# Optimization experiments

Measured on AMD Instinct MI355X. Metric: run time of the kernel, lower is better.

Reference implementation:

```python
import jax, jax.numpy as jnp
import numpy as np

REGION_INDEX = [[3,0,1,2,4],[7,8,9,10,11],[5,6],[13,12],[14,15,23,24,32,33],[22,21,31,30,40,39],[16,17,18,19,20],[25,26,27,28,29],[34,35,36,37,38],[41,42],[49,48],[43,44,45,46,47],[50,51,57],[56,55,61],[52,53,54],[58,59,60]]
INPUT_SIZE = 5
HIDDEN = 100
REGIONS = 16


def setup_inputs() -> dict:
    key = jax.random.key(0)
    ks = jax.random.split(key, 5)
    features = jax.random.normal(ks[0], (128, 256, 62, INPUT_SIZE), dtype=jnp.float32)
    s = 1.0 / np.sqrt(HIDDEN)  # PyTorch LSTM init scale
    # dir 0 = forward, dir 1 = reverse
    w_ih = jax.random.uniform(ks[1], (REGIONS, 2, 4 * HIDDEN, INPUT_SIZE), jnp.float32, -s, s)
    w_hh = jax.random.uniform(ks[2], (REGIONS, 2, 4 * HIDDEN, HIDDEN), jnp.float32, -s, s)
    b_ih = jax.random.uniform(ks[3], (REGIONS, 2, 4 * HIDDEN), jnp.float32, -s, s)
    b_hh = jax.random.uniform(ks[4], (REGIONS, 2, 4 * HIDDEN), jnp.float32, -s, s)
    return {"features": features, "w_ih": w_ih, "w_hh": w_hh, "b_ih": b_ih, "b_hh": b_hh}


def _lstm_last(x, Wih, Whh, bih, bhh):
    # x: (N, L, I) -> final hidden state h_{L-1}: (N, H). PyTorch gate order i,f,g,o.
    N = x.shape[0]
    H = Whh.shape[1]
    bias = bih + bhh

    def step(carry, xt):
        h, c = carry
        g = xt @ Wih.T + h @ Whh.T + bias
        i, f, gg, o = jnp.split(g, 4, axis=-1)
        c = jax.nn.sigmoid(f) * c + jax.nn.sigmoid(i) * jnp.tanh(gg)
        h = jax.nn.sigmoid(o) * jnp.tanh(c)
        return (h, c), None

    h0 = jnp.zeros((N, H), x.dtype)
    (h, _), _ = jax.lax.scan(step, (h0, h0), jnp.swapaxes(x, 0, 1))
    return h


def _forward(features, w_ih, w_hh, b_ih, b_hh):
    # flatten (B, T, 62, 5) -> (N, 62, 5)
    x = features.reshape(-1, features.shape[2], features.shape[3])
    outs = []
    for r in range(REGIONS):
        idx = jnp.asarray(REGION_INDEX[r])
        xr = x[:, idx, :]  # (N, L_r, 5)
        # forward-direction hidden at last timestep
        h_f = _lstm_last(xr, w_ih[r, 0], w_hh[r, 0], b_ih[r, 0], b_hh[r, 0])
        # reverse-direction output at last position == one step on x[:, -1] from zero state
        h_b = _lstm_last(xr[:, -1:, :], w_ih[r, 1], w_hh[r, 1], b_ih[r, 1], b_hh[r, 1])
        outs.append(jnp.concatenate([h_f, h_b], axis=-1))  # (N, 2H)
    return jnp.stack(outs, axis=1)  # (N, 16, 2H)


def reference(features, w_ih, w_hh, b_ih, b_hh):
    return _forward(features, w_ih, w_hh, b_ih, b_hh)
```

## Files before the change

kernel.cpp:

```cpp
#include <hip/hip_runtime.h>


typedef _Float16 f16;
typedef _Float16 half8 __attribute__((ext_vector_type(8)));
typedef float floatx4 __attribute__((ext_vector_type(4)));

#define FEAT_STRIDE 310
#define AST 136
#define OST 104

__constant__ int c_pos[16][6] = {
 {3,0,1,2,4,0},{7,8,9,10,11,0},{5,6,0,0,0,0},{13,12,0,0,0,0},
 {14,15,23,24,32,33},{22,21,31,30,40,39},{16,17,18,19,20,0},{25,26,27,28,29,0},
 {34,35,36,37,38,0},{41,42,0,0,0,0},{49,48,0,0,0,0},{43,44,45,46,47,0},
 {50,51,57,0,0,0},{56,55,61,0,0,0},{52,53,54,0,0,0},{58,59,60,0,0,0}};
__constant__ int c_len[16] = {5,5,2,2,6,6,5,5,5,2,2,5,3,3,3,3};

__device__ __forceinline__ float sigf(float x) {
  return __builtin_amdgcn_rcpf(1.f + __builtin_amdgcn_exp2f(-1.44269504088896f * x));
}
__device__ __forceinline__ float tanhf_fast(float x) {
  return 1.f - 2.f * __builtin_amdgcn_rcpf(1.f + __builtin_amdgcn_exp2f(2.88539008177793f * x));
}

__global__ __launch_bounds__(256) void prep_kernel(
    const float* __restrict__ w_ih, const float* __restrict__ w_hh,
    const float* __restrict__ b_ih, const float* __restrict__ b_hh,
    f16* __restrict__ wp)
{
  int id = blockIdx.x * 256 + threadIdx.x;
  if (id >= 16 * 400 * 128) return;
  int k = id & 127;
  int rowN = (id >> 7) % 400;
  int r = (id >> 7) / 400;
  int j = rowN >> 2, g = rowN & 3;
  int orig = (r * 2 + 0) * 400 + g * 100 + j;
  float v;
  if (k < 100)       v = w_hh[orig * 100 + k];
  else if (k < 105)  v = w_ih[orig * 5 + (k - 100)];
  else if (k == 105) v = b_ih[orig] + b_hh[orig];
  else               v = 0.f;
  wp[id] = (f16)v;
}

__global__ __launch_bounds__(320, 3) void fwd_kernel(
    const float* __restrict__ feat, const f16* __restrict__ wp,
    float* __restrict__ out)
{
  __shared__ __align__(16) float smem[32 * OST];
  f16* Alds = (f16*)smem;

  const int bx = blockIdx.x;
  const int r  = bx >> 10;
  const int n0 = (bx & 1023) << 5;
  const int tid  = threadIdx.x;
  const int wave = tid >> 6;
  const int lane = tid & 63;
  const int quad = lane >> 4;
  const int l15  = lane & 15;
  const int T = c_len[r];

  half8 wf[5][4];
  {
    const f16* wr = wp + (size_t)r * 400 * 128;
    #pragma unroll
    for (int tn = 0; tn < 5; ++tn) {
      int row = 16 * (5 * wave + tn) + l15;
      #pragma unroll
      for (int kf = 0; kf < 4; ++kf)
        wf[tn][kf] = *(const half8*)(wr + row * 128 + 32 * kf + 8 * quad);
    }
  }

  for (int i = tid; i < 32 * 64; i += 320) {
    int m = i >> 6, kw = i & 63;
    ((unsigned int*)smem)[m * (AST / 2) + kw] = (kw == 52) ? 0x3C000000u : 0u;
  }

  float xv[6];
  const int xm = tid & 31, xs = tid >> 5;
  if (tid < 160) {
    const float* fb = feat + (size_t)(n0 + xm) * FEAT_STRIDE + xs;
    #pragma unroll
    for (int tt = 0; tt < 6; ++tt)
      if (tt < T) xv[tt] = fb[c_pos[r][tt] * 5];
  }
  __syncthreads();
  if (tid < 160) Alds[xm * AST + 100 + xs] = (f16)xv[0];
  __syncthreads();

  float creg[2][5];
  #pragma unroll
  for (int mt = 0; mt < 2; ++mt)
    #pragma unroll
    for (int tn = 0; tn < 5; ++tn) creg[mt][tn] = 0.f;

  for (int t = 0; t < T; ++t) {
    float hreg[2][5];
    #pragma unroll
    for (int mt = 0; mt < 2; ++mt) {
      half8 bf[4];
      #pragma unroll
      for (int kf = 0; kf < 4; ++kf)
        bf[kf] = *(const half8*)(Alds + (16 * mt + l15) * AST + 32 * kf + 8 * quad);
      #pragma unroll
      for (int tn = 0; tn < 5; ++tn) {
        floatx4 acc = {0.f, 0.f, 0.f, 0.f};
        #pragma unroll
        for (int kf = 0; kf < 4; ++kf)
          acc = __builtin_amdgcn_mfma_f32_16x16x32_f16(wf[tn][kf], bf[kf], acc, 0, 0, 0);
        float ig = sigf(acc[0]);
        float fg = sigf(acc[1]);
        float gg = tanhf_fast(acc[2]);
        float og = sigf(acc[3]);
        float cn = fg * creg[mt][tn] + ig * gg;
        creg[mt][tn] = cn;
        hreg[mt][tn] = og * tanhf_fast(cn);
      }
    }
    __syncthreads();
    if (t + 1 < T) {
      #pragma unroll
      for (int mt = 0; mt < 2; ++mt)
        #pragma unroll
        for (int tn = 0; tn < 5; ++tn) {
          int j = 4 * (5 * wave + tn) + quad;
          Alds[(16 * mt + l15) * AST + j] = (f16)hreg[mt][tn];
        }
      if (tid < 160) Alds[xm * AST + 100 + xs] = (f16)xv[t + 1];
    } else {
      #pragma unroll
      for (int mt = 0; mt < 2; ++mt)
        #pragma unroll
        for (int tn = 0; tn < 5; ++tn) {
          int j = 4 * (5 * wave + tn) + quad;
          smem[(16 * mt + l15) * OST + j] = hreg[mt][tn];
        }
    }
    __syncthreads();
  }

  #pragma unroll
  for (int it = 0; it < 3; ++it) {
    int idx = tid + it * 320;
    if (idx < 800) {
      int m = idx / 25, ch = idx - m * 25;
      floatx4 v = *(const floatx4*)(smem + m * OST + ch * 4);
      *(floatx4*)(out + (size_t)(n0 + m) * 3200 + r * 200 + ch * 4) = v;
    }
  }
}

__global__ __launch_bounds__(256) void bwd_kernel(
    const float* __restrict__ feat, const float* __restrict__ w_ih,
    const float* __restrict__ b_ih, const float* __restrict__ b_hh,
    float* __restrict__ out)
{
  __shared__ float wg[300 * 7];
  __shared__ float xs[128 * 5];
  const int bx = blockIdx.x;
  const int r  = bx >> 8;
  const int n0 = (bx & 255) << 7;
  const int tid = threadIdx.x;
  const int pos = c_pos[r][c_len[r] - 1];

  for (int i = tid; i < 2100; i += 256) {
    int row = i / 7, c = i - row * 7;
    int q = row / 100, jj = row - q * 100;
    int qq = (q == 0) ? 0 : (q + 1);
    int orig = (r * 2 + 1) * 400 + qq * 100 + jj;
    float v = 0.f;
    if (c < 5)       v = w_ih[orig * 5 + c];
    else if (c == 5) v = b_ih[orig] + b_hh[orig];
    wg[i] = v;
  }
  for (int i = tid; i < 640; i += 256) {
    int nl = i / 5, s = i - nl * 5;
    xs[i] = feat[(size_t)(n0 + nl) * FEAT_STRIDE + pos * 5 + s];
  }
  __syncthreads();

  for (int idx = tid; idx < 12800; idx += 256) {
    int nl = idx / 100, jj = idx - nl * 100;
    const float* xp = xs + nl * 5;
    float x0 = xp[0], x1 = xp[1], x2 = xp[2], x3 = xp[3], x4 = xp[4];
    const float* wi = wg + jj * 7;
    const float* wc = wg + (100 + jj) * 7;
    const float* wo = wg + (200 + jj) * 7;
    float gi = wi[5] + wi[0]*x0 + wi[1]*x1 + wi[2]*x2 + wi[3]*x3 + wi[4]*x4;
    float gc = wc[5] + wc[0]*x0 + wc[1]*x1 + wc[2]*x2 + wc[3]*x3 + wc[4]*x4;
    float go = wo[5] + wo[0]*x0 + wo[1]*x1 + wo[2]*x2 + wo[3]*x3 + wo[4]*x4;
    float c = sigf(gi) * tanhf_fast(gc);
    float h = sigf(go) * tanhf_fast(c);
    out[(size_t)(n0 + nl) * 3200 + r * 200 + 100 + jj] = h;
  }
}

extern "C" void kernel_launch(void* const* d_in, const int* in_sizes, int n_in,
                              void* d_out, int out_size, void* d_ws, size_t ws_size,
                              hipStream_t stream) {
  const float* feat = (const float*)d_in[0];
  const float* w_ih = (const float*)d_in[1];
  const float* w_hh = (const float*)d_in[2];
  const float* b_ih = (const float*)d_in[3];
  const float* b_hh = (const float*)d_in[4];
  float* out = (float*)d_out;
  f16* wp = (f16*)d_ws;

  prep_kernel<<<3200, 256, 0, stream>>>(w_ih, w_hh, b_ih, b_hh, wp);
  fwd_kernel<<<16384, 320, 0, stream>>>(feat, wp, out);
  bwd_kernel<<<4096, 256, 0, stream>>>(feat, w_ih, b_ih, b_hh, out);
}
```

Before: 1.178 ms.

## Double-buffer LSTM hidden state in LDS and double rows per block

```diff
diff --git a/kernel.cpp b/kernel.cpp
--- a/kernel.cpp
+++ b/kernel.cpp
@@ -7,6 +7,7 @@
 
 #define FEAT_STRIDE 310
 #define AST 136
+#define ASZ (64 * AST)
 #define OST 104
 
 __constant__ int c_pos[16][6] = {
@@ -47,12 +48,12 @@
     const float* __restrict__ feat, const f16* __restrict__ wp,
     float* __restrict__ out)
 {
-  __shared__ __align__(16) float smem[32 * OST];
-  f16* Alds = (f16*)smem;
+  __shared__ __align__(16) f16 Abuf[2 * ASZ];
+  float* smemf = (float*)Abuf;
 
   const int bx = blockIdx.x;
-  const int r  = bx >> 10;
-  const int n0 = (bx & 1023) << 5;
+  const int r  = bx >> 9;
+  const int n0 = (bx & 511) << 6;
   const int tid  = threadIdx.x;
   const int wave = tid >> 6;
   const int lane = tid & 63;
@@ -72,82 +73,96 @@
     }
   }
 
-  for (int i = tid; i < 32 * 64; i += 320) {
-    int m = i >> 6, kw = i & 63;
-    ((unsigned int*)smem)[m * (AST / 2) + kw] = (kw == 52) ? 0x3C000000u : 0u;
+  for (int i = tid; i < 2 * 64 * 64; i += 320) {
+    int buf = i >> 12;
+    int rem = i & 4095;
+    int m = rem >> 6, kw = rem & 63;
+    ((unsigned int*)Abuf)[buf * (ASZ / 2) + m * (AST / 2) + kw] =
+        (kw == 52) ? 0x3C000000u : 0u;
   }
 
   float xv[6];
-  const int xm = tid & 31, xs = tid >> 5;
-  if (tid < 160) {
+  const int xm = tid & 63, xs = tid >> 6;
+  {
     const float* fb = feat + (size_t)(n0 + xm) * FEAT_STRIDE + xs;
     #pragma unroll
     for (int tt = 0; tt < 6; ++tt)
       if (tt < T) xv[tt] = fb[c_pos[r][tt] * 5];
   }
   __syncthreads();
-  if (tid < 160) Alds[xm * AST + 100 + xs] = (f16)xv[0];
+  Abuf[xm * AST + 100 + xs] = (f16)xv[0];
   __syncthreads();
 
-  float creg[2][5];
+  float creg[4][5];
   #pragma unroll
-  for (int mt = 0; mt < 2; ++mt)
+  for (int mt = 0; mt < 4; ++mt)
     #pragma unroll
     for (int tn = 0; tn < 5; ++tn) creg[mt][tn] = 0.f;
 
   for (int t = 0; t < T; ++t) {
-    float hreg[2][5];
-    #pragma unroll
-    for (int mt = 0; mt < 2; ++mt) {
-      half8 bf[4];
-      #pragma unroll
-      for (int kf = 0; kf < 4; ++kf)
-        bf[kf] = *(const half8*)(Alds + (16 * mt + l15) * AST + 32 * kf + 8 * quad);
-      #pragma unroll
-      for (int tn = 0; tn < 5; ++tn) {
-        floatx4 acc = {0.f, 0.f, 0.f, 0.f};
+    const f16* Acur = Abuf + (t & 1) * ASZ;
+    f16* Anxt = Abuf + ((t + 1) & 1) * ASZ;
+
+    if (t + 1 < T) {
+      #pragma unroll
+      for (int mt = 0; mt < 4; ++mt) {
+        half8 bf[4];
         #pragma unroll
         for (int kf = 0; kf < 4; ++kf)
-          acc = __builtin_amdgcn_mfma_f32_16x16x32_f16(wf[tn][kf], bf[kf], acc, 0, 0, 0);
-        float ig = sigf(acc[0]);
-        float fg = sigf(acc[1]);
-        float gg = tanhf_fast(acc[2]);
-        float og = sigf(acc[3]);
-        float cn = fg * creg[mt][tn] + ig * gg;
-        creg[mt][tn] = cn;
-        hreg[mt][tn] = og * tanhf_fast(cn);
+          bf[kf] = *(const half8*)(Acur + (16 * mt + l15) * AST + 32 * kf + 8 * quad);
+        #pragma unroll
+        for (int tn = 0; tn < 5; ++tn) {
+          floatx4 acc = {0.f, 0.f, 0.f, 0.f};
+          #pragma unroll
+          for (int kf = 0; kf < 4; ++kf)
+            acc = __builtin_amdgcn_mfma_f32_16x16x32_f16(wf[tn][kf], bf[kf], acc, 0, 0, 0);
+          float ig = sigf(acc[0]);
+          float fg = sigf(acc[1]);
+          float gg = tanhf_fast(acc[2]);
+          float og = sigf(acc[3]);
+          float cn = fg * creg[mt][tn] + ig * gg;
+          creg[mt][tn] = cn;
+          int j = 4 * (5 * wave + tn) + quad;
+          Anxt[(16 * mt + l15) * AST + j] = (f16)(og * tanhf_fast(cn));
+        }
       }
+      Anxt[xm * AST + 100 + xs] = (f16)xv[t + 1];
+      __syncthreads();
+    } else {
+      half8 bfa[4][4];
+      #pragma unroll
+      for (int mt = 0; mt < 4; ++mt)
+        #pragma unroll
+        for (int kf = 0; kf < 4; ++kf)
+          bfa[mt][kf] = *(const half8*)(Acur + (16 * mt + l15) * AST + 32 * kf + 8 * quad);
+      __syncthreads();
+      #pragma unroll
+      for (int mt = 0; mt < 4; ++mt) {
+        #pragma unroll
+        for (int tn = 0; tn < 5; ++tn) {
+          floatx4 acc = {0.f, 0.f, 0.f, 0.f};
+          #pragma unroll
+          for (int kf = 0; kf < 4; ++kf)
+            acc = __builtin_amdgcn_mfma_f32_16x16x32_f16(wf[tn][kf], bfa[mt][kf], acc, 0, 0, 0);
+          float ig = sigf(acc[0]);
+          float fg = sigf(acc[1]);
+          float gg = tanhf_fast(acc[2]);
+          float og = sigf(acc[3]);
+          float cn = fg * creg[mt][tn] + ig * gg;
+          int j = 4 * (5 * wave + tn) + quad;
+          smemf[(16 * mt + l15) * OST + j] = og * tanhf_fast(cn);
+        }
+      }
+      __syncthreads();
     }
-    __syncthreads();
-    if (t + 1 < T) {
-      #pragma unroll
-      for (int mt = 0; mt < 2; ++mt)
-        #pragma unroll
-        for (int tn = 0; tn < 5; ++tn) {
-          int j = 4 * (5 * wave + tn) + quad;
-          Alds[(16 * mt + l15) * AST + j] = (f16)hreg[mt][tn];
-        }
-      if (tid < 160) Alds[xm * AST + 100 + xs] = (f16)xv[t + 1];
-    } else {
-      #pragma unroll
-      for (int mt = 0; mt < 2; ++mt)
-        #pragma unroll
-        for (int tn = 0; tn < 5; ++tn) {
-          int j = 4 * (5 * wave + tn) + quad;
-          smem[(16 * mt + l15) * OST + j] = hreg[mt][tn];
-        }
-    }
-    __syncthreads();
   }
 
   #pragma unroll
-  for (int it = 0; it < 3; ++it) {
+  for (int it = 0; it < 5; ++it) {
     int idx = tid + it * 320;
-    if (idx < 800) {
-      int m = idx / 25, ch = idx - m * 25;
-      floatx4 v = *(const floatx4*)(smem + m * OST + ch * 4);
-      *(floatx4*)(out + (size_t)(n0 + m) * 3200 + r * 200 + ch * 4) = v;
-    }
+    int m = idx / 25, ch = idx - m * 25;
+    floatx4 v = *(const floatx4*)(smemf + m * OST + ch * 4);
+    *(floatx4*)(out + (size_t)(n0 + m) * 3200 + r * 200 + ch * 4) = v;
   }
 }
 
@@ -208,6 +223,6 @@
   f16* wp = (f16*)d_ws;
 
   prep_kernel<<<3200, 256, 0, stream>>>(w_ih, w_hh, b_ih, b_hh, wp);
-  fwd_kernel<<<16384, 320, 0, stream>>>(feat, wp, out);
+  fwd_kernel<<<8192, 320, 0, stream>>>(feat, wp, out);
   bwd_kernel<<<4096, 256, 0, stream>>>(feat, w_ih, b_ih, b_hh, out);
 }
```

Result: slower. 1.442 ms (+22.5%).
